# Optimization experiments

Measured on AMD Instinct MI355X. Metric: run time of the kernel, lower is better.

The kernel has to match this reference:

```python
import jax, jax.numpy as jnp
import numpy as np

ROT_DIM = 32
THETA = 10000.0
HEAD_SIZE = 192


def _rope(t):
    # t: [B, T, D]; rotate first ROT_DIM features with interleaved-pair RoPE
    T = t.shape[1]
    inv_freq = 1.0 / (THETA ** (jnp.arange(0, ROT_DIM, 2, dtype=jnp.float32) / ROT_DIM))  # [16]
    freqs = jnp.arange(T, dtype=jnp.float32)[:, None] * inv_freq[None, :]  # [T,16]
    freqs = jnp.repeat(freqs, 2, axis=-1)  # [T,32], each freq repeated for the pair
    cos = jnp.cos(freqs).astype(t.dtype)
    sin = jnp.sin(freqs).astype(t.dtype)
    x = t[..., :ROT_DIM]
    x1 = x[..., 0::2]
    x2 = x[..., 1::2]
    rot_half = jnp.stack([-x2, x1], axis=-1).reshape(x.shape)  # interleave (-x2, x1)
    rotated = x * cos + rot_half * sin
    return jnp.concatenate([rotated, t[..., ROT_DIM:]], axis=-1)


def setup_inputs() -> dict:
    key = jax.random.key(0)
    k1, k2, k3, k4 = jax.random.split(key, 4)
    B, T, C, H = 64, 512, 768, HEAD_SIZE
    x = jax.random.normal(k1, (B, T, C), dtype=jnp.float32)
    s = 1.0 / np.sqrt(C)
    Wq = jax.random.normal(k2, (C, H), dtype=jnp.float32) * s
    Wk = jax.random.normal(k3, (C, H), dtype=jnp.float32) * s
    Wv = jax.random.normal(k4, (C, H), dtype=jnp.float32) * s
    return {"x": x, "Wq": Wq, "Wk": Wk, "Wv": Wv}


def reference(x, Wq, Wk, Wv):
    B, T, C = x.shape
    q = x @ Wq  # [B,T,H]
    k = x @ Wk
    v = x @ Wv
    q = _rope(q)
    k = _rope(k)
    scale = k.shape[-1] ** -0.5
    scores = jnp.einsum('bqh,bkh->bqk', q, k) * scale  # [B,T,T]
    causal = jnp.tril(jnp.ones((T, T), dtype=bool))
    scores = jnp.where(causal[None, :, :], scores, -jnp.inf)
    weight = jax.nn.softmax(scores, axis=-1)
    # dropout is identity at eval time
    out = jnp.einsum('bqk,bkh->bqh', weight, v)  # [B,T,H]
    return out
```

## Files before the change

### kernel.cpp

```cpp
#include <hip/hip_runtime.h>
#include <cstdint>

typedef __attribute__((ext_vector_type(8))) short short8;
typedef __attribute__((ext_vector_type(4))) float floatx4;

__device__ __forceinline__ unsigned short f2bf(float f) {
  uint32_t u = __builtin_bit_cast(uint32_t, f);
  u += 0x7fffu + ((u >> 16) & 1u);
  return (unsigned short)(u >> 16);
}
__device__ __forceinline__ uint32_t pkbf(float lo, float hi) {
  uint32_t a = __builtin_bit_cast(uint32_t, lo) + 0x8000u;
  uint32_t b = __builtin_bit_cast(uint32_t, hi) + 0x8000u;
  return __builtin_amdgcn_perm(b, a, 0x07060302);
}
__device__ __forceinline__ void gll16(const void* g, void* l) {
  __builtin_amdgcn_global_load_lds(
      (const __attribute__((address_space(1))) unsigned int*)g,
      (__attribute__((address_space(3))) unsigned int*)l, 16, 0, 0);
}

__global__ void prep_w_kernel(const float* __restrict__ Wq,
                              const float* __restrict__ Wk,
                              const float* __restrict__ Wv,
                              unsigned short* __restrict__ Wt) {
  int id = blockIdx.x * 256 + threadIdx.x;
  int bz = id / 18432, rem = id - bz * 18432;
  int kb = rem / 768, s = rem - kb * 768;
  int row = s >> 2, cs = s & 3;
  int c = cs ^ ((row >> 1) & 3);
  const float* W = (bz == 0) ? Wq : (bz == 1) ? Wk : Wv;
  int k0 = kb * 32 + c * 8;
  unsigned short v[8];
#pragma unroll
  for (int e = 0; e < 8; ++e) v[e] = f2bf(W[(size_t)(k0 + e) * 192 + row]);
  uint4 o;
  o.x = v[0] | ((uint32_t)v[1] << 16);
  o.y = v[2] | ((uint32_t)v[3] << 16);
  o.z = v[4] | ((uint32_t)v[5] << 16);
  o.w = v[6] | ((uint32_t)v[7] << 16);
  *(uint4*)(Wt + (size_t)id * 8) = o;
}

__global__ __launch_bounds__(256, 5) void proj_kernel(
    const float* __restrict__ x, const unsigned short* __restrict__ Wt,
    unsigned short* __restrict__ q_ws, unsigned short* __restrict__ k_ws,
    unsigned short* __restrict__ v_ws) {
  __shared__ __align__(16) unsigned short A_lds[2][64 * 32];
  __shared__ __align__(16) unsigned short B_lds[2][192 * 32];
  const int tid = threadIdx.x;
  const int w = tid >> 6, l = tid & 63, quad = l >> 4, ln = l & 15;
  const int wr = w & 1, wc = w >> 1;
  const int m0 = blockIdx.x * 64;
  const int bz = blockIdx.y;

  const int arow = tid >> 2, ac = tid & 3;
  const int aslot = ((ac ^ ((arow >> 1) & 3)) << 4);
  const float* xp = x + (size_t)(m0 + arow) * 768 + ac * 8;
  const unsigned short* wimg = Wt + (size_t)bz * 18432 * 8;

  const int fq = ((quad ^ ((ln >> 1) & 3)) << 4);

  floatx4 acc[2][6];
#pragma unroll
  for (int mi = 0; mi < 2; ++mi)
#pragma unroll
    for (int nj = 0; nj < 6; ++nj) acc[mi][nj] = floatx4{0.f, 0.f, 0.f, 0.f};

  float4 a0x, a0y;

#define LOADA(K0)                                  \
  do {                                             \
    a0x = *(const float4*)(xp + (K0));             \
    a0y = *(const float4*)(xp + (K0) + 4);         \
  } while (0)
#define STAGEA(BUF)                                               \
  do {                                                            \
    uint4 ap;                                                     \
    ap.x = pkbf(a0x.x, a0x.y);                                    \
    ap.y = pkbf(a0x.z, a0x.w);                                    \
    ap.z = pkbf(a0y.x, a0y.y);                                    \
    ap.w = pkbf(a0y.z, a0y.w);                                    \
    *(uint4*)((char*)&A_lds[BUF][0] + arow * 64 + aslot) = ap;    \
  } while (0)
#define LOADB(KB, BUF)                                               \
  do {                                                               \
    const unsigned short* src = wimg + (size_t)(KB) * 6144;          \
    char* dstb = (char*)&B_lds[BUF][0];                              \
    _Pragma("unroll") for (int it = 0; it < 3; ++it)                 \
        gll16(src + (it * 256 + tid) * 8, dstb + (it * 256 + tid) * 16); \
  } while (0)
#define PCOMPUTE(BUF)                                                            \
  do {                                                                           \
    short8 af0 = *(const short8*)((const char*)&A_lds[BUF][0] +                  \
                                  (wr * 32 + ln) * 64 + fq);                     \
    short8 af1 = *(const short8*)((const char*)&A_lds[BUF][0] +                  \
                                  (wr * 32 + 16 + ln) * 64 + fq);                \
    _Pragma("unroll") for (int nj = 0; nj < 6; ++nj) {                           \
      short8 bf = *(const short8*)((const char*)&B_lds[BUF][0] +                 \
                                   (wc * 96 + nj * 16 + ln) * 64 + fq);          \
      acc[0][nj] = __builtin_amdgcn_mfma_f32_16x16x32_bf16(af0, bf, acc[0][nj],  \
                                                           0, 0, 0);             \
      acc[1][nj] = __builtin_amdgcn_mfma_f32_16x16x32_bf16(af1, bf, acc[1][nj],  \
                                                           0, 0, 0);             \
    }                                                                            \
  } while (0)

  LOADB(0, 0);
  LOADA(0);
  STAGEA(0);
  LOADA(32);
  __syncthreads();

#pragma unroll 2
  for (int kb = 0; kb < 24; ++kb) {
    const int cur = kb & 1, nxt = cur ^ 1;
    if (kb < 23) {
      LOADB(kb + 1, nxt);
      STAGEA(nxt);
    }
    if (kb < 22) LOADA((kb + 2) * 32);
    PCOMPUTE(cur);
    __syncthreads();
  }
#undef LOADA
#undef STAGEA
#undef LOADB
#undef PCOMPUTE

  const float R_LG = 0.8304820237218406f;
#define ROPE2(V0, V1, TPOS)                                         \
  do {                                                              \
    float i0 = (float)(ln >> 1);                                    \
    float f0 = exp2f(-i0 * R_LG);                                   \
    float f1 = exp2f(-(i0 + 8.0f) * R_LG);                          \
    float s0, c0, s1, c1;                                           \
    sincosf((float)(TPOS)*f0, &s0, &c0);                            \
    sincosf((float)(TPOS)*f1, &s1, &c1);                            \
    float p0 = __shfl_xor(V0, 1), p1 = __shfl_xor(V1, 1);           \
    V0 = (ln & 1) ? (V0 * c0 + p0 * s0) : (V0 * c0 - p0 * s0);      \
    V1 = (ln & 1) ? (V1 * c1 + p1 * s1) : (V1 * c1 - p1 * s1);      \
  } while (0)

  if (bz < 2) {
    unsigned short* dst = (bz == 0) ? q_ws : k_ws;
    if (wc == 0) {
#pragma unroll
      for (int mi = 0; mi < 2; ++mi)
#pragma unroll
        for (int r = 0; r < 4; ++r) {
          int row_g = m0 + wr * 32 + mi * 16 + quad * 4 + r;
          int t_pos = row_g & 511;
          float v0 = acc[mi][0][r], v1 = acc[mi][1][r];
          ROPE2(v0, v1, t_pos);
          dst[(size_t)row_g * 192 + ln] = f2bf(v0);
          dst[(size_t)row_g * 192 + 16 + ln] = f2bf(v1);
#pragma unroll
          for (int nj = 2; nj < 6; ++nj)
            dst[(size_t)row_g * 192 + nj * 16 + ln] = f2bf(acc[mi][nj][r]);
        }
    } else {
#pragma unroll
      for (int mi = 0; mi < 2; ++mi)
#pragma unroll
        for (int r = 0; r < 4; ++r) {
          int row_g = m0 + wr * 32 + mi * 16 + quad * 4 + r;
#pragma unroll
          for (int nj = 0; nj < 6; ++nj)
            dst[(size_t)row_g * 192 + 96 + nj * 16 + ln] = f2bf(acc[mi][nj][r]);
        }
    }
  } else {
    const int dbase = wc * 96;
#pragma unroll
    for (int mi = 0; mi < 2; ++mi) {
      int rb = m0 + wr * 32 + mi * 16 + quad * 4;
      int bb = rb >> 9, t = rb & 511;
#pragma unroll
      for (int nj = 0; nj < 6; ++nj) {
        ushort4 pv;
        pv.x = f2bf(acc[mi][nj][0]);
        pv.y = f2bf(acc[mi][nj][1]);
        pv.z = f2bf(acc[mi][nj][2]);
        pv.w = f2bf(acc[mi][nj][3]);
        *(ushort4*)&v_ws[((size_t)bb * 192 + dbase + nj * 16 + ln) * 512 + t] = pv;
      }
    }
  }
#undef ROPE2
}

__global__ __launch_bounds__(256) void attn_kernel(
    const unsigned short* __restrict__ q_ws, const unsigned short* __restrict__ k_ws,
    const unsigned short* __restrict__ v_ws, float* __restrict__ out) {
  __shared__ __align__(16) unsigned short K_lds[64 * 200];
  __shared__ __align__(16) unsigned short V_lds[192 * 72];
  __shared__ __align__(16) unsigned short P_lds[4][16 * 72];
  const int tid = threadIdx.x;
  const int w = tid >> 6, l = tid & 63, quad = l >> 4, ln = l & 15;
  const int b = blockIdx.y;
  const int qt = (blockIdx.y < 32) ? blockIdx.x : 7 - blockIdx.x;
  const int q0 = qt * 64;

  short8 qf[6];
  {
    const unsigned short* qp =
        q_ws + (size_t)(b * 512 + q0 + w * 16 + ln) * 192 + quad * 8;
#pragma unroll
    for (int kk = 0; kk < 6; ++kk) qf[kk] = *(const short8*)(qp + kk * 32);
  }

  float m_i[4], l_i[4];
  floatx4 o[12];
#pragma unroll
  for (int r = 0; r < 4; ++r) { m_i[r] = -1e30f; l_i[r] = 0.f; }
#pragma unroll
  for (int nt = 0; nt < 12; ++nt) o[nt] = floatx4{0.f, 0.f, 0.f, 0.f};
  const float sm_scale = 0.07216878364870323f;

  for (int kt = 0; kt <= qt; ++kt) {
    const int k0 = kt * 64;
    __syncthreads();
#pragma unroll
    for (int it = 0; it < 6; ++it) {
      int idx = it * 256 + tid;
      int row = idx / 24, c = idx - row * 24;
      uint4 v = *(const uint4*)(k_ws + (size_t)(b * 512 + k0 + row) * 192 + c * 8);
      *(uint4*)&K_lds[row * 200 + c * 8] = v;
    }
#pragma unroll
    for (int it = 0; it < 6; ++it) {
      int idx = it * 256 + tid;
      int row = idx >> 3, c = idx & 7;
      uint4 v = *(const uint4*)(v_ws + (size_t)(b * 192 + row) * 512 + k0 + c * 8);
      *(uint4*)&V_lds[row * 72 + c * 8] = v;
    }
    __syncthreads();

    float s[4][4];
    __builtin_amdgcn_s_setprio(1);
#pragma unroll
    for (int nt = 0; nt < 4; ++nt) {
      floatx4 sa = floatx4{0.f, 0.f, 0.f, 0.f};
#pragma unroll
      for (int kk = 0; kk < 6; ++kk) {
        short8 kf = *(const short8*)&K_lds[(nt * 16 + ln) * 200 + kk * 32 + quad * 8];
        sa = __builtin_amdgcn_mfma_f32_16x16x32_bf16(qf[kk], kf, sa, 0, 0, 0);
      }
#pragma unroll
      for (int r = 0; r < 4; ++r) s[nt][r] = sa[r] * sm_scale;
    }
    __builtin_amdgcn_s_setprio(0);
    if (kt == qt) {
#pragma unroll
      for (int nt = 0; nt < 4; ++nt)
#pragma unroll
        for (int r = 0; r < 4; ++r)
          if (nt * 16 + ln > w * 16 + quad * 4 + r) s[nt][r] = -1e30f;
    }
    float alpha[4];
#pragma unroll
    for (int r = 0; r < 4; ++r) {
      float mx = fmaxf(fmaxf(s[0][r], s[1][r]), fmaxf(s[2][r], s[3][r]));
      mx = fmaxf(mx, __shfl_xor(mx, 1));
      mx = fmaxf(mx, __shfl_xor(mx, 2));
      mx = fmaxf(mx, __shfl_xor(mx, 4));
      mx = fmaxf(mx, __shfl_xor(mx, 8));
      float mnew = fmaxf(m_i[r], mx);
      alpha[r] = __expf(m_i[r] - mnew);
      float sum = 0.f;
#pragma unroll
      for (int nt = 0; nt < 4; ++nt) {
        s[nt][r] = __expf(s[nt][r] - mnew);
        sum += s[nt][r];
      }
      sum += __shfl_xor(sum, 1);
      sum += __shfl_xor(sum, 2);
      sum += __shfl_xor(sum, 4);
      sum += __shfl_xor(sum, 8);
      l_i[r] = l_i[r] * alpha[r] + sum;
      m_i[r] = mnew;
    }
#pragma unroll
    for (int nt = 0; nt < 12; ++nt)
#pragma unroll
      for (int r = 0; r < 4; ++r) o[nt][r] *= alpha[r];

#pragma unroll
    for (int nt = 0; nt < 4; ++nt)
#pragma unroll
      for (int r = 0; r < 4; ++r)
        P_lds[w][(quad * 4 + r) * 72 + nt * 16 + ln] = f2bf(s[nt][r]);
    __asm__ volatile("s_waitcnt lgkmcnt(0)" ::: "memory");

    __builtin_amdgcn_s_setprio(1);
#pragma unroll
    for (int ks = 0; ks < 2; ++ks) {
      short8 pf = *(const short8*)&P_lds[w][ln * 72 + ks * 32 + quad * 8];
#pragma unroll
      for (int nt = 0; nt < 12; ++nt) {
        short8 vf = *(const short8*)&V_lds[(nt * 16 + ln) * 72 + ks * 32 + quad * 8];
        o[nt] = __builtin_amdgcn_mfma_f32_16x16x32_bf16(pf, vf, o[nt], 0, 0, 0);
      }
    }
    __builtin_amdgcn_s_setprio(0);
  }

#pragma unroll
  for (int r = 0; r < 4; ++r) {
    float inv = 1.0f / l_i[r];
    size_t rowoff = (size_t)(b * 512 + q0 + w * 16 + quad * 4 + r) * 192;
#pragma unroll
    for (int nt = 0; nt < 12; ++nt)
      out[rowoff + nt * 16 + ln] = o[nt][r] * inv;
  }
}

extern "C" void kernel_launch(void* const* d_in, const int* in_sizes, int n_in,
                              void* d_out, int out_size, void* d_ws, size_t ws_size,
                              hipStream_t stream) {
  const float* x = (const float*)d_in[0];
  const float* Wq = (const float*)d_in[1];
  const float* Wk = (const float*)d_in[2];
  const float* Wv = (const float*)d_in[3];
  float* out = (float*)d_out;

  char* ws = (char*)d_ws;
  const size_t QKV_BYTES = (size_t)64 * 512 * 192 * 2;
  unsigned short* q_ws = (unsigned short*)(ws);
  unsigned short* k_ws = (unsigned short*)(ws + QKV_BYTES);
  unsigned short* v_ws = (unsigned short*)(ws + 2 * QKV_BYTES);
  unsigned short* Wt = (unsigned short*)(ws + 3 * QKV_BYTES);

  hipLaunchKernelGGL(prep_w_kernel, dim3(216), dim3(256), 0, stream, Wq, Wk, Wv, Wt);
  hipLaunchKernelGGL(proj_kernel, dim3(512, 3), dim3(256), 0, stream, x, Wt, q_ws, k_ws, v_ws);
  hipLaunchKernelGGL(attn_kernel, dim3(8, 64), dim3(256), 0, stream, q_ws, k_ws, v_ws, out);
}
```

Before: 236.5 us.

## Triple-buffer projection GEMM with manual waitcnt and one barrier per step

Converts the QKV projection main loop from double to triple buffering of A and B in LDS. The x loads are prefetched three stages ahead, and `__syncthreads` is replaced by an explicit `s_waitcnt vmcnt(N)` plus `s_barrier`, so the DMA for later stages stays in flight while the current stage computes. The goal is to hide global-memory latency and remove the full drain at each barrier. In exchange it uses more LDS and registers and lowers launch bounds from 5 to 3 blocks per CU, which reduces occupancy.

```diff
diff --git a/kernel.cpp b/kernel.cpp
--- a/kernel.cpp
+++ b/kernel.cpp
@@ -42,12 +42,12 @@
   *(uint4*)(Wt + (size_t)id * 8) = o;
 }
 
-__global__ __launch_bounds__(256, 5) void proj_kernel(
+__global__ __launch_bounds__(256, 3) void proj_kernel(
     const float* __restrict__ x, const unsigned short* __restrict__ Wt,
     unsigned short* __restrict__ q_ws, unsigned short* __restrict__ k_ws,
     unsigned short* __restrict__ v_ws) {
-  __shared__ __align__(16) unsigned short A_lds[2][64 * 32];
-  __shared__ __align__(16) unsigned short B_lds[2][192 * 32];
+  __shared__ __align__(16) unsigned short A_lds[3][64 * 32];
+  __shared__ __align__(16) unsigned short B_lds[3][192 * 32];
   const int tid = threadIdx.x;
   const int w = tid >> 6, l = tid & 63, quad = l >> 4, ln = l & 15;
   const int wr = w & 1, wc = w >> 1;
@@ -67,37 +67,40 @@
 #pragma unroll
     for (int nj = 0; nj < 6; ++nj) acc[mi][nj] = floatx4{0.f, 0.f, 0.f, 0.f};
 
-  float4 a0x, a0y;
-
-#define LOADA(K0)                                  \
+  float4 ax0, ay0, ax1, ay1, ax2, ay2;
+
+#define LOADA(S, K0)                               \
   do {                                             \
-    a0x = *(const float4*)(xp + (K0));             \
-    a0y = *(const float4*)(xp + (K0) + 4);         \
-  } while (0)
-#define STAGEA(BUF)                                               \
+    ax##S = *(const float4*)(xp + (K0));           \
+    ay##S = *(const float4*)(xp + (K0) + 4);       \
+  } while (0)
+#define STAGEA(S, AB)                                             \
   do {                                                            \
     uint4 ap;                                                     \
-    ap.x = pkbf(a0x.x, a0x.y);                                    \
-    ap.y = pkbf(a0x.z, a0x.w);                                    \
-    ap.z = pkbf(a0y.x, a0y.y);                                    \
-    ap.w = pkbf(a0y.z, a0y.w);                                    \
-    *(uint4*)((char*)&A_lds[BUF][0] + arow * 64 + aslot) = ap;    \
-  } while (0)
-#define LOADB(KB, BUF)                                               \
-  do {                                                               \
-    const unsigned short* src = wimg + (size_t)(KB) * 6144;          \
-    char* dstb = (char*)&B_lds[BUF][0];                              \
-    _Pragma("unroll") for (int it = 0; it < 3; ++it)                 \
-        gll16(src + (it * 256 + tid) * 8, dstb + (it * 256 + tid) * 16); \
-  } while (0)
-#define PCOMPUTE(BUF)                                                            \
+    ap.x = pkbf(ax##S.x, ax##S.y);                                \
+    ap.y = pkbf(ax##S.z, ax##S.w);                                \
+    ap.z = pkbf(ay##S.x, ay##S.y);                                \
+    ap.w = pkbf(ay##S.z, ay##S.w);                                \
+    *(uint4*)((char*)&A_lds[AB][0] + arow * 64 + aslot) = ap;     \
+  } while (0)
+#define DMAB(KB1, BB)                                             \
+  do {                                                            \
+    const unsigned short* src = wimg + (size_t)(KB1)*6144;        \
+    char* dstb = (char*)&B_lds[BB][0];                            \
+    gll16(src + tid * 8, dstb + tid * 16);                        \
+    gll16(src + (256 + tid) * 8, dstb + (256 + tid) * 16);        \
+    gll16(src + (512 + tid) * 8, dstb + (512 + tid) * 16);        \
+  } while (0)
+#define WAITBAR(N)                                                          \
+  asm volatile("s_waitcnt vmcnt(" #N ") lgkmcnt(0)\n\ts_barrier" ::: "memory")
+#define PCOMPUTE(C)                                                              \
   do {                                                                           \
-    short8 af0 = *(const short8*)((const char*)&A_lds[BUF][0] +                  \
+    short8 af0 = *(const short8*)((const char*)&A_lds[C][0] +                    \
                                   (wr * 32 + ln) * 64 + fq);                     \
-    short8 af1 = *(const short8*)((const char*)&A_lds[BUF][0] +                  \
+    short8 af1 = *(const short8*)((const char*)&A_lds[C][0] +                    \
                                   (wr * 32 + 16 + ln) * 64 + fq);                \
     _Pragma("unroll") for (int nj = 0; nj < 6; ++nj) {                           \
-      short8 bf = *(const short8*)((const char*)&B_lds[BUF][0] +                 \
+      short8 bf = *(const short8*)((const char*)&B_lds[C][0] +                   \
                                    (wc * 96 + nj * 16 + ln) * 64 + fq);          \
       acc[0][nj] = __builtin_amdgcn_mfma_f32_16x16x32_bf16(af0, bf, acc[0][nj],  \
                                                            0, 0, 0);             \
@@ -105,28 +108,39 @@
                                                            0, 0, 0);             \
     }                                                                            \
   } while (0)
-
-  LOADB(0, 0);
-  LOADA(0);
-  STAGEA(0);
-  LOADA(32);
-  __syncthreads();
-
-#pragma unroll 2
-  for (int kb = 0; kb < 24; ++kb) {
-    const int cur = kb & 1, nxt = cur ^ 1;
-    if (kb < 23) {
-      LOADB(kb + 1, nxt);
-      STAGEA(nxt);
-    }
-    if (kb < 22) LOADA((kb + 2) * 32);
-    PCOMPUTE(cur);
-    __syncthreads();
-  }
+#define BODY(KB, C, P)            \
+  do {                            \
+    STAGEA(P, P);                 \
+    DMAB((KB) + 1, P);            \
+    LOADA(C, ((KB) + 3) * 32);    \
+    WAITBAR(7);                   \
+    PCOMPUTE(C);                  \
+  } while (0)
+
+  DMAB(0, 0);
+  LOADA(0, 0);
+  LOADA(1, 32);
+  LOADA(2, 64);
+  STAGEA(0, 0);
+
+  BODY(0, 0, 1);
+  for (int t = 1; t <= 16; t += 3) {
+    BODY(t, 1, 2);
+    BODY(t + 1, 2, 0);
+    BODY(t + 2, 0, 1);
+  }
+  BODY(19, 1, 2);
+  BODY(20, 2, 0);
+  { STAGEA(1, 1); DMAB(22, 1); WAITBAR(5); PCOMPUTE(0); }
+  { STAGEA(2, 2); DMAB(23, 2); WAITBAR(3); PCOMPUTE(1); }
+  { WAITBAR(0); PCOMPUTE(2); }
+
 #undef LOADA
 #undef STAGEA
-#undef LOADB
+#undef DMAB
+#undef WAITBAR
 #undef PCOMPUTE
+#undef BODY
 
   const float R_LG = 0.8304820237218406f;
 #define ROPE2(V0, V1, TPOS)                                         \
```

Result: faster. 222.5 us (-5.9%).
